# Kernel tuning notes

Measured on AMD Instinct MI355X. Metric: run time of the kernel, lower is better.

Reference implementation:

```python
import jax, jax.numpy as jnp
import numpy as np

# Fixed geometry from the module's voxel_dict
VOXEL = np.array([0.32, 0.32, 6.0], dtype=np.float32)
PC_MIN = np.array([-74.88, -74.88, -2.0], dtype=np.float32)
PC_MAX = np.array([74.88, 74.88, 4.0], dtype=np.float32)
NX, NY, NZ = 468, 468, 1          # round((max-min)/voxel) per axis
CANVAS = NZ * NY * NX             # 219024 voxels (batch_size = 1)
OFFSET = VOXEL / 2.0 + PC_MIN     # x/y/z_offset from __init__


def setup_inputs() -> dict:
    key = jax.random.key(0)
    k1, k2, k3, k4 = jax.random.split(key, 4)
    N = 400000
    # points uniformly inside the point-cloud range (dynamic voxelization keeps all)
    xyz = jax.random.uniform(k1, (N, 3), dtype=jnp.float32) * (PC_MAX - PC_MIN) * 0.999 + PC_MIN
    extra = jax.random.normal(k2, (N, 2), dtype=jnp.float32)
    points = jnp.concatenate([xyz, extra], axis=1)          # [N, 5]
    W1 = jax.random.normal(k3, (11, 64), dtype=jnp.float32) * 0.05
    W2 = jax.random.normal(k4, (128, 64), dtype=jnp.float32) * 0.05
    return {"points": points, "W1": W1, "W2": W2}


def _flat_voxel_index(xyz):
    # dynamic voxelization: integer voxel coord per point, (z, y, x) ordering
    c = jnp.floor((xyz - PC_MIN) / VOXEL).astype(jnp.int32)
    cx = jnp.clip(c[:, 0], 0, NX - 1)
    cy = jnp.clip(c[:, 1], 0, NY - 1)
    cz = jnp.clip(c[:, 2], 0, NZ - 1)
    flat = cz * (NY * NX) + cy * NX + cx                    # canvas index as in map_voxel_center_to_point
    return flat, cx, cy, cz


def reference(points, W1, W2):
    xyz = points[:, :3]
    flat, cx, cy, cz = _flat_voxel_index(xyz)

    # DynamicScatter mean (cluster_scatter)
    cnt = jax.ops.segment_sum(jnp.ones((points.shape[0],), jnp.float32), flat, num_segments=CANVAS)
    vsum = jax.ops.segment_sum(points, flat, num_segments=CANVAS)
    vmean = vsum / jnp.maximum(cnt, 1.0)[:, None]           # [CANVAS, 5]
    pmean = vmean[flat]                                     # gather voxel mean to points

    f_cluster = xyz - pmean[:, :3]
    centers = jnp.stack([cx, cy, cz], axis=1).astype(jnp.float32) * VOXEL + OFFSET
    f_center = xyz - centers
    features = jnp.concatenate([points, f_cluster, f_center], axis=-1)   # [N, 11]

    occ = (cnt > 0)[:, None]

    # PFN layer 1: Linear(bias=False) + ReLU, then scatter-max to voxels
    pf1 = jax.nn.relu(features @ W1)                        # [N, 64]
    v1 = jax.ops.segment_max(pf1, flat, num_segments=CANVAS)
    v1 = jnp.where(occ, v1, 0.0)                            # zero empty voxels (replaces -inf)

    # gather voxel max back to points, concat, PFN layer 2
    feat2 = jnp.concatenate([pf1, v1[flat]], axis=1)        # [N, 128]
    pf2 = jax.nn.relu(feat2 @ W2)                           # [N, 64]
    v2 = jax.ops.segment_max(pf2, flat, num_segments=CANVAS)
    v2 = jnp.where(occ, v2, 0.0)                            # [CANVAS, 64] dense voxel features
    return v2
```

## Files before the change

### kernel.cpp

```cpp
#include <hip/hip_runtime.h>

#define NXc 468
#define NYc 468
#define CANVASc (468 * 468)
#define NPTS 400000
#define RUN 16
#define NRUNS (NPTS / RUN)
#define GPTS ((NPTS + 255) / 256)
#define GVOX ((CANVASc + 255) / 256)
#define GSEAM ((NRUNS + 255) / 256)

#define PCMIN_X (-74.88f)
#define PCMIN_Y (-74.88f)
#define VOX_X 0.32f
#define VOX_Y 0.32f
#define OFF_X (-74.72f)
#define OFF_Y (-74.72f)
#define OFF_Z (1.0f)

typedef __attribute__((ext_vector_type(8))) short v8s;
typedef __attribute__((ext_vector_type(4))) float v4f;

static_assert(sizeof(__bf16) == 2, "bf16 must be 2 bytes");

__device__ __forceinline__ int rli(int x, int p) {
    return __builtin_amdgcn_readlane(x, p);
}

__device__ __forceinline__ void split8(const float* f, v8s& h, v8s& l) {
    #pragma unroll
    for (int i = 0; i < 8; i += 2) {
        __bf16 h0 = (__bf16)f[i];
        __bf16 h1 = (__bf16)f[i + 1];
        h[i]     = __builtin_bit_cast(short, h0);
        h[i + 1] = __builtin_bit_cast(short, h1);
        float l0 = f[i]     - (float)h0;
        float l1 = f[i + 1] - (float)h1;
        l[i]     = __builtin_bit_cast(short, (__bf16)l0);
        l[i + 1] = __builtin_bit_cast(short, (__bf16)l1);
    }
}

__device__ __forceinline__ int voxel_cell(float x, float y, int& cx, int& cy) {
    cx = (int)floorf((x - PCMIN_X) / VOX_X);
    cy = (int)floorf((y - PCMIN_Y) / VOX_Y);
    cx = min(max(cx, 0), NXc - 1);
    cy = min(max(cy, 0), NYc - 1);
    return cy * NXc + cx;
}

__device__ __forceinline__ void kw_body(int tid,
                                        const float* __restrict__ W1,
                                        const float* __restrict__ W2,
                                        v8s* __restrict__ w1frag,
                                        v8s* __restrict__ w2frag) {
    if (tid < 1024) {
        int f = tid >> 6, lane = tid & 63;
        int t = f >> 2, c = f & 3;
        int q = lane >> 4, n = lane & 15;
        float v[8];
        #pragma unroll
        for (int i = 0; i < 8; i++) v[i] = W2[(c * 32 + q * 8 + i) * 64 + t * 16 + n];
        v8s h, l;
        split8(v, h, l);
        w2frag[(f * 2 + 0) * 64 + lane] = h;
        w2frag[(f * 2 + 1) * 64 + lane] = l;
    } else if (tid < 1280) {
        int f = (tid - 1024) >> 6, lane = (tid - 1024) & 63;
        int q = lane >> 4, n = lane & 15;
        float v[8];
        #pragma unroll
        for (int i = 0; i < 8; i++) {
            int k = q * 8 + i;
            v[i] = (k < 11) ? W1[k * 64 + f * 16 + n] : 0.f;
        }
        v8s h, l;
        split8(v, h, l);
        w1frag[(f * 2 + 0) * 64 + lane] = h;
        w1frag[(f * 2 + 1) * 64 + lane] = l;
    }
}

__global__ __launch_bounds__(256) void k_stats(const float* __restrict__ pts,
                                               int* __restrict__ cnt,
                                               const float* __restrict__ W1,
                                               const float* __restrict__ W2,
                                               v8s* __restrict__ w1frag,
                                               v8s* __restrict__ w2frag) {
    int b = blockIdx.x;
    if (b >= GPTS) {
        kw_body((b - GPTS) * 256 + threadIdx.x, W1, W2, w1frag, w2frag);
        return;
    }
    int i = b * 256 + threadIdx.x;
    if (i >= NPTS) return;
    float x = pts[i * 5 + 0], y = pts[i * 5 + 1];
    int cx, cy;
    int fl = voxel_cell(x, y, cx, cy);
    atomicAdd(&cnt[fl], 1);
}

__global__ __launch_bounds__(256) void k_alloc(const int* __restrict__ cnt,
                                               int* __restrict__ cursor,
                                               int* __restrict__ gcur) {
    int v = blockIdx.x * 256 + threadIdx.x;
    int lane = threadIdx.x & 63;
    int c = (v < CANVASc) ? cnt[v] : 0;
    int scan = c;
    #pragma unroll
    for (int off = 1; off < 64; off <<= 1) {
        int t = __shfl_up(scan, off, 64);
        if (lane >= off) scan += t;
    }
    int total = __shfl(scan, 63, 64);
    int base = 0;
    if (lane == 0 && total > 0) base = atomicAdd(gcur, total);
    base = __shfl(base, 0, 64);
    if (v < CANVASc) cursor[v] = base + scan - c;
}

__device__ __forceinline__ void gather_pt(const float* __restrict__ pts, int pi,
                                          float4& A, float& e1) {
    const float* pp = pts + (size_t)pi * 5;
    __builtin_memcpy(&A, pp, 16);
    e1 = pp[4];
}

__global__ __launch_bounds__(256) void k_scatter(const float* __restrict__ pts,
                                                 int* __restrict__ cursor,
                                                 float4* __restrict__ pos4,
                                                 float* __restrict__ e1b,
                                                 int* __restrict__ cellb) {
    int i = blockIdx.x * 256 + threadIdx.x;
    if (i >= NPTS) return;
    float4 A; float e1;
    gather_pt(pts, i, A, e1);
    int cx, cy;
    int fl = voxel_cell(A.x, A.y, cx, cy);
    int pos = atomicAdd(&cursor[fl], 1);
    pos4[pos] = A;
    e1b[pos] = e1;
    cellb[pos] = cx | (cy << 16);
}

__global__ __launch_bounds__(256) void kV(const int* __restrict__ cnt,
                                          const int* __restrict__ cursor,
                                          const float4* __restrict__ pos4,
                                          const int* __restrict__ cellb,
                                          float4* __restrict__ vmean4,
                                          float4* __restrict__ v14,
                                          float4* __restrict__ out4) {
    int b = blockIdx.x;
    if (b >= GVOX) {
        int w = (b - GVOX) * 256 + threadIdx.x;
        if (w == 0 || w >= NRUNS) return;
        int bb = w * RUN;
        int ca = cellb[bb - 1], cb = cellb[bb];
        if (ca != cb) return;
        int cx = ca & 0xFFFF, cy = ca >> 16;
        int va = cy * NXc + cx;
        float4 z = make_float4(0.f, 0.f, 0.f, 0.f);
        float4* o = out4 + (size_t)va * 16;
        float4* q = v14 + (size_t)va * 16;
        #pragma unroll
        for (int i = 0; i < 16; i++) { o[i] = z; q[i] = z; }
        return;
    }
    int v = b * 256 + threadIdx.x;
    if (v >= CANVASc) return;
    int c = cnt[v];
    if (c == 0) {
        float4 z = make_float4(0.f, 0.f, 0.f, 0.f);
        float4* o = out4 + (size_t)v * 16;
        #pragma unroll
        for (int i = 0; i < 16; i++) o[i] = z;
        return;
    }
    int start = cursor[v] - c;
    float sx = 0.f, sy = 0.f, sz = 0.f;
    for (int i = 0; i < c; i++) {
        float4 p = pos4[start + i];
        sx += p.x; sy += p.y; sz += p.z;
    }
    float inv = 1.0f / (float)c;
    vmean4[v] = make_float4(sx * inv, sy * inv, sz * inv, 0.f);
}

struct PtRegs {
    float4 A;
    float  e1, fcx, fcy, fcz;
    float  mx, my, mz;
    int    vx;
};
__device__ __forceinline__ PtRegs load_pt(const float4* __restrict__ pos4,
                                          const float* __restrict__ e1b,
                                          const int* __restrict__ cellb,
                                          const float4* __restrict__ vmean4,
                                          int base, int j) {
    PtRegs r;
    r.A = make_float4(0.f, 0.f, 0.f, 0.f);
    r.e1 = r.fcx = r.fcy = r.fcz = r.mx = r.my = r.mz = 0.f;
    r.vx = -1;
    int idx = -1;
    if (j < RUN) idx = base + j;
    else if (j == 16) idx = (base + RUN < NPTS) ? base + RUN : -1;
    else if (j == 17) idx = base - 1;
    if (idx >= 0) {
        int cell = cellb[idx];
        int cx = cell & 0xFFFF, cy = cell >> 16;
        int vv = cy * NXc + cx;
        r.vx = vv;
        if (j < RUN) {
            float4 A = pos4[idx];
            r.A = A;
            r.e1 = e1b[idx];
            r.fcx = A.x - (cx * VOX_X + OFF_X);
            r.fcy = A.y - (cy * VOX_Y + OFF_Y);
            r.fcz = A.z - OFF_Z;
            float4 m = vmean4[vv];
            r.mx = m.x; r.my = m.y; r.mz = m.z;
        }
    }
    return r;
}

#define PSTR 68

__device__ __forceinline__ void phase1_mfma(float (*s_pf)[PSTR], const PtRegs& P,
                                            const v8s* __restrict__ w1frag, int j) {
    if (j < RUN) {
        float* row = s_pf[j];
        row[0] = P.A.x; row[1] = P.A.y; row[2] = P.A.z; row[3] = P.A.w; row[4] = P.e1;
        row[5] = P.A.x - P.mx; row[6] = P.A.y - P.my; row[7] = P.A.z - P.mz;
        row[8] = P.fcx; row[9] = P.fcy; row[10] = P.fcz;
        #pragma unroll
        for (int t = 11; t < 16; t++) row[t] = 0.f;
    }
    __builtin_amdgcn_wave_barrier();

    const int m = j & 15, q = j >> 4;
    v8s fh = {0,0,0,0,0,0,0,0}, fl_ = {0,0,0,0,0,0,0,0};
    if (q < 2) {
        float f8[8];
        #pragma unroll
        for (int i = 0; i < 8; i++) f8[i] = s_pf[m][q * 8 + i];
        split8(f8, fh, fl_);
    }
    v4f d[4];
    #pragma unroll
    for (int t = 0; t < 4; t++) {
        v8s bh = w1frag[(t * 2 + 0) * 64 + j];
        v8s bl = w1frag[(t * 2 + 1) * 64 + j];
        v4f acc = {0.f, 0.f, 0.f, 0.f};
        acc = __builtin_amdgcn_mfma_f32_16x16x32_bf16(fh,  bh, acc, 0, 0, 0);
        acc = __builtin_amdgcn_mfma_f32_16x16x32_bf16(fl_, bh, acc, 0, 0, 0);
        acc = __builtin_amdgcn_mfma_f32_16x16x32_bf16(fh,  bl, acc, 0, 0, 0);
        d[t] = acc;
    }
    __builtin_amdgcn_wave_barrier();
    #pragma unroll
    for (int t = 0; t < 4; t++)
        #pragma unroll
        for (int r = 0; r < 4; r++)
            s_pf[q * 4 + r][t * 16 + m] = fmaxf(d[t][r], 0.f);
    __builtin_amdgcn_wave_barrier();
}

__global__ __launch_bounds__(256) void kA(const float4* __restrict__ pos4,
                                          const float* __restrict__ e1b,
                                          const int* __restrict__ cellb,
                                          const float4* __restrict__ vmean4,
                                          const v8s* __restrict__ w1frag,
                                          float* __restrict__ v1) {
    __shared__ float s_pf[4][RUN][PSTR];
    int wslot = threadIdx.x >> 6;
    int wave = blockIdx.x * 4 + wslot;
    int j = threadIdx.x & 63;
    int base = wave * RUN;

    PtRegs P = load_pt(pos4, e1b, cellb, vmean4, base, j);
    phase1_mfma(s_pf[wslot], P, w1frag, j);

    const int first = rli(P.vx, 0), last = rli(P.vx, RUN - 1);
    const bool firstExt = (rli(P.vx, 17) == first);
    const bool lastExt  = (rli(P.vx, 16) == last);
    int vprev = first;
    float smax = 0.f;
    for (int p = 0; p < RUN; p++) {
        int vp = rli(P.vx, p);
        if (vp != vprev) {
            size_t o = (size_t)vprev * 64 + j;
            bool ua = (vprev == first && firstExt) || (vprev == last && lastExt);
            if (ua) atomicMax((int*)v1 + o, __float_as_int(smax));
            else v1[o] = smax;
            vprev = vp; smax = 0.f;
        }
        smax = fmaxf(smax, s_pf[wslot][p][j]);
    }
    {
        size_t o = (size_t)vprev * 64 + j;
        bool ua = (vprev == first && firstExt) || (vprev == last && lastExt);
        if (ua) atomicMax((int*)v1 + o, __float_as_int(smax));
        else v1[o] = smax;
    }
}

__global__ __launch_bounds__(256) void kB(const float4* __restrict__ pos4,
                                          const float* __restrict__ e1b,
                                          const int* __restrict__ cellb,
                                          const float4* __restrict__ vmean4,
                                          const v8s* __restrict__ w1frag,
                                          const v8s* __restrict__ w2frag,
                                          const float* __restrict__ v1,
                                          float* __restrict__ out) {
    __shared__ float s_pf[4][RUN][PSTR];
    int wslot = threadIdx.x >> 6;
    int wave = blockIdx.x * 4 + wslot;
    int j = threadIdx.x & 63;
    int base = wave * RUN;

    PtRegs P = load_pt(pos4, e1b, cellb, vmean4, base, j);

    const int m = j & 15, q = j >> 4;

    int vx_m = __builtin_amdgcn_ds_bpermute(m << 2, P.vx);
    float vf[16];
    {
        const float* vr = v1 + (size_t)vx_m * 64 + q * 8;
        #pragma unroll
        for (int c = 0; c < 2; c++)
            #pragma unroll
            for (int i = 0; i < 8; i++) vf[c * 8 + i] = vr[c * 32 + i];
    }

    phase1_mfma(s_pf[wslot], P, w1frag, j);

    v8s ah[4], al[4];
    #pragma unroll
    for (int c = 0; c < 2; c++) {
        float f[8];
        #pragma unroll
        for (int i = 0; i < 8; i++) f[i] = s_pf[wslot][m][c * 32 + q * 8 + i];
        split8(f, ah[c], al[c]);
    }
    split8(vf + 0, ah[2], al[2]);
    split8(vf + 8, ah[3], al[3]);
    __builtin_amdgcn_wave_barrier();

    #pragma unroll
    for (int t = 0; t < 4; t++) {
        v8s bh[4], bl[4];
        #pragma unroll
        for (int c = 0; c < 4; c++) {
            bh[c] = w2frag[((t * 4 + c) * 2 + 0) * 64 + j];
            bl[c] = w2frag[((t * 4 + c) * 2 + 1) * 64 + j];
        }
        v4f acc = {0.f, 0.f, 0.f, 0.f};
        #pragma unroll
        for (int c = 0; c < 4; c++) {
            acc = __builtin_amdgcn_mfma_f32_16x16x32_bf16(ah[c], bh[c], acc, 0, 0, 0);
            acc = __builtin_amdgcn_mfma_f32_16x16x32_bf16(al[c], bh[c], acc, 0, 0, 0);
            acc = __builtin_amdgcn_mfma_f32_16x16x32_bf16(ah[c], bl[c], acc, 0, 0, 0);
        }
        #pragma unroll
        for (int r = 0; r < 4; r++) s_pf[wslot][q * 4 + r][t * 16 + m] = acc[r];
    }
    __builtin_amdgcn_wave_barrier();

    const int first = rli(P.vx, 0), last = rli(P.vx, RUN - 1);
    const bool firstExt = (rli(P.vx, 17) == first);
    const bool lastExt  = (rli(P.vx, 16) == last);
    int vprev = first;
    float smax = -3.4e38f;
    for (int p = 0; p < RUN; p++) {
        int vp = rli(P.vx, p);
        if (vp != vprev) {
            float r = fmaxf(smax, 0.f);
            size_t o = (size_t)vprev * 64 + j;
            bool ua = (vprev == first && firstExt) || (vprev == last && lastExt);
            if (ua) atomicMax((int*)out + o, __float_as_int(r));
            else out[o] = r;
            vprev = vp; smax = -3.4e38f;
        }
        smax = fmaxf(smax, s_pf[wslot][p][j]);
    }
    {
        float r = fmaxf(smax, 0.f);
        size_t o = (size_t)vprev * 64 + j;
        bool ua = (vprev == first && firstExt) || (vprev == last && lastExt);
        if (ua) atomicMax((int*)out + o, __float_as_int(r));
        else out[o] = r;
    }
}

extern "C" void kernel_launch(void* const* d_in, const int* in_sizes, int n_in,
                              void* d_out, int out_size, void* d_ws, size_t ws_size,
                              hipStream_t stream) {
    const float* pts = (const float*)d_in[0];
    const float* W1  = (const float*)d_in[1];
    const float* W2  = (const float*)d_in[2];
    float* out = (float*)d_out;

    float4* vmean4 = (float4*)d_ws;
    float*  v1     = (float*)(vmean4 + CANVASc);
    float4* pos4   = (float4*)(v1 + (size_t)CANVASc * 64);
    float*  e1b    = (float*)(pos4 + NPTS);
    int*    cellb  = (int*)(e1b + NPTS);
    v8s*    w2frag = (v8s*)(cellb + NPTS);
    v8s*    w1frag = w2frag + 2048;
    int*    cnt    = (int*)(w1frag + 512);
    int*    gcur   = cnt + CANVASc;
    int*    cursor = gcur + 1;

    hipMemsetAsync(cnt, 0, (size_t)(CANVASc + 1) * 4, stream);

    k_stats  <<<GPTS + 5, 256, 0, stream>>>(pts, cnt, W1, W2, w1frag, w2frag);
    k_alloc  <<<GVOX, 256, 0, stream>>>(cnt, cursor, gcur);
    k_scatter<<<GPTS, 256, 0, stream>>>(pts, cursor, pos4, e1b, cellb);
    kV       <<<GVOX + GSEAM, 256, 0, stream>>>(cnt, cursor, pos4, cellb,
                                                vmean4, (float4*)v1, (float4*)out);
    kA       <<<NRUNS / 4, 256, 0, stream>>>(pos4, e1b, cellb, vmean4, w1frag, v1);
    kB       <<<NRUNS / 4, 256, 0, stream>>>(pos4, e1b, cellb, vmean4, w1frag,
                                             w2frag, v1, out);
}
```

Baseline: 242.2 us.

## Skip layer-1 global round trip for voxels wholly inside a wave's run

kA now returns early for waves whose run has no voxel crossing into neighbouring runs, and writes only the boundary voxels via atomicMax. kB computes each point's segment bounds with a ballot and takes the voxel max of layer-1 features from shared memory for interior voxels, reading v1 from global memory only for boundary voxels. This cuts v1 stores and loads and most kA MFMA work. kB gains ballot, clz/ctz and a per-lane segment loop, and kA's early exit leaves interior v1 entries unwritten, so correctness depends on kB never reading them.

Measured after the change: 236.6 us. 2.3% less time.

```diff
diff --git a/kernel.cpp b/kernel.cpp
--- a/kernel.cpp
+++ b/kernel.cpp
@@ -279,29 +279,28 @@
     int base = wave * RUN;
 
     PtRegs P = load_pt(pos4, e1b, cellb, vmean4, base, j);
-    phase1_mfma(s_pf[wslot], P, w1frag, j);
 
     const int first = rli(P.vx, 0), last = rli(P.vx, RUN - 1);
     const bool firstExt = (rli(P.vx, 17) == first);
     const bool lastExt  = (rli(P.vx, 16) == last);
+    if (!firstExt && !lastExt) return;
+
+    phase1_mfma(s_pf[wslot], P, w1frag, j);
+
     int vprev = first;
     float smax = 0.f;
     for (int p = 0; p < RUN; p++) {
         int vp = rli(P.vx, p);
         if (vp != vprev) {
-            size_t o = (size_t)vprev * 64 + j;
             bool ua = (vprev == first && firstExt) || (vprev == last && lastExt);
-            if (ua) atomicMax((int*)v1 + o, __float_as_int(smax));
-            else v1[o] = smax;
+            if (ua) atomicMax((int*)v1 + (size_t)vprev * 64 + j, __float_as_int(smax));
             vprev = vp; smax = 0.f;
         }
         smax = fmaxf(smax, s_pf[wslot][p][j]);
     }
     {
-        size_t o = (size_t)vprev * 64 + j;
         bool ua = (vprev == first && firstExt) || (vprev == last && lastExt);
-        if (ua) atomicMax((int*)v1 + o, __float_as_int(smax));
-        else v1[o] = smax;
+        if (ua) atomicMax((int*)v1 + (size_t)vprev * 64 + j, __float_as_int(smax));
     }
 }
 
@@ -323,9 +322,22 @@
 
     const int m = j & 15, q = j >> 4;
 
+    const int first = rli(P.vx, 0), last = rli(P.vx, RUN - 1);
+    const bool firstExt = (rli(P.vx, 17) == first);
+    const bool lastExt  = (rli(P.vx, 16) == last);
+
     int vx_m = __builtin_amdgcn_ds_bpermute(m << 2, P.vx);
+    int vx_prev = __shfl_up(P.vx, 1, 64);
+    unsigned long long B =
+        __ballot((j < RUN) && ((j == 0) || (P.vx != vx_prev)));
+    int s_seg = 63 - __builtin_clzll(B & ((2ULL << m) - 1ULL));
+    int e_seg = m + 1 + (int)__builtin_ctzll((B | (1ULL << RUN)) >> (m + 1));
+    const bool ext_m = (vx_m == first && firstExt) || (vx_m == last && lastExt);
+
+    phase1_mfma(s_pf[wslot], P, w1frag, j);
+
     float vf[16];
-    {
+    if (ext_m) {
         const float* vr = v1 + (size_t)vx_m * 64 + q * 8;
         #pragma unroll
         for (int c = 0; c < 2; c++)
@@ -333,8 +345,6 @@
             for (int i = 0; i < 8; i++) vf[c * 8 + i] = vr[c * 32 + i];
     }
 
-    phase1_mfma(s_pf[wslot], P, w1frag, j);
-
     v8s ah[4], al[4];
     #pragma unroll
     for (int c = 0; c < 2; c++) {
@@ -342,6 +352,25 @@
         #pragma unroll
         for (int i = 0; i < 8; i++) f[i] = s_pf[wslot][m][c * 32 + q * 8 + i];
         split8(f, ah[c], al[c]);
+    }
+    if (!ext_m) {
+        #pragma unroll
+        for (int i = 0; i < 16; i++) vf[i] = 0.f;
+        for (int p = s_seg; p < e_seg; p++) {
+            const float* row = s_pf[wslot][p];
+            float4 a0 = *(const float4*)&row[q * 8];
+            float4 a1 = *(const float4*)&row[q * 8 + 4];
+            float4 b0 = *(const float4*)&row[32 + q * 8];
+            float4 b1 = *(const float4*)&row[32 + q * 8 + 4];
+            vf[0] = fmaxf(vf[0], a0.x);  vf[1] = fmaxf(vf[1], a0.y);
+            vf[2] = fmaxf(vf[2], a0.z);  vf[3] = fmaxf(vf[3], a0.w);
+            vf[4] = fmaxf(vf[4], a1.x);  vf[5] = fmaxf(vf[5], a1.y);
+            vf[6] = fmaxf(vf[6], a1.z);  vf[7] = fmaxf(vf[7], a1.w);
+            vf[8] = fmaxf(vf[8], b0.x);  vf[9] = fmaxf(vf[9], b0.y);
+            vf[10] = fmaxf(vf[10], b0.z); vf[11] = fmaxf(vf[11], b0.w);
+            vf[12] = fmaxf(vf[12], b1.x); vf[13] = fmaxf(vf[13], b1.y);
+            vf[14] = fmaxf(vf[14], b1.z); vf[15] = fmaxf(vf[15], b1.w);
+        }
     }
     split8(vf + 0, ah[2], al[2]);
     split8(vf + 8, ah[3], al[3]);
@@ -367,9 +396,6 @@
     }
     __builtin_amdgcn_wave_barrier();
 
-    const int first = rli(P.vx, 0), last = rli(P.vx, RUN - 1);
-    const bool firstExt = (rli(P.vx, 17) == first);
-    const bool lastExt  = (rli(P.vx, 16) == last);
     int vprev = first;
     float smax = -3.4e38f;
     for (int p = 0; p < RUN; p++) {
```
